# Optimization experiments

Hardware: AMD Instinct MI355X
Metric: run time of the kernel (lower is better)

## Reference

```python
import jax, jax.numpy as jnp
import numpy as np

FEATURE_DIM = 512
HIDDEN_DIM = 512
N_HEADS = 8
HEAD_DIM = HIDDEN_DIM // N_HEADS
MAX_LEN = 5000
GAMMA = 0.5  # gaussian relative-position bias width
LN_EPS = 1e-5


def make_pe(d_model, max_len):
    # sinusoidal positional encoding buffer, as in PositionalEncoding.__init__
    pos = jnp.arange(max_len, dtype=jnp.float32)[:, None]
    div = jnp.exp(jnp.arange(0, d_model, 2, dtype=jnp.float32) * (-np.log(10000.0) / d_model))
    ang = pos * div  # [max_len, d_model/2]
    pe = jnp.zeros((max_len, d_model), dtype=jnp.float32)
    pe = pe.at[:, 0::2].set(jnp.sin(ang)).at[:, 1::2].set(jnp.cos(ang))
    return pe


def setup_inputs() -> dict:
    key = jax.random.key(0)
    k_x, k_q, k_k, k_v = jax.random.split(key, 4)
    xavier = np.sqrt(6.0 / (FEATURE_DIM + HEAD_DIM))  # xavier_uniform over last two dims
    return {
        "data_window": jax.random.normal(k_x, (1, 2048, FEATURE_DIM), dtype=jnp.float32),
        "W_query": jax.random.uniform(k_q, (N_HEADS, FEATURE_DIM, HEAD_DIM), jnp.float32, -xavier, xavier),
        "W_key": jax.random.uniform(k_k, (N_HEADS, FEATURE_DIM, HEAD_DIM), jnp.float32, -xavier, xavier),
        "W_value": jax.random.uniform(k_v, (N_HEADS, FEATURE_DIM, HEAD_DIM), jnp.float32, -xavier, xavier),
        "ln_gamma": jnp.ones((FEATURE_DIM,), dtype=jnp.float32),
        "ln_beta": jnp.zeros((FEATURE_DIM,), dtype=jnp.float32),
    }


def reference(data_window, W_query, W_key, W_value, ln_gamma, ln_beta):
    B, S, F = data_window.shape
    temperature = 1.0

    # LayerNorm over feature dim
    mu = jnp.mean(data_window, axis=-1, keepdims=True)
    var = jnp.mean(jnp.square(data_window - mu), axis=-1, keepdims=True)
    x = (data_window - mu) * jax.lax.rsqrt(var + LN_EPS) * ln_gamma + ln_beta

    # positional encoding, exactly as original: x + pe[:x.shape[0]] (requires B==1)
    pe = make_pe(FEATURE_DIM, MAX_LEN)
    x = x + pe[:B]  # [B,F] broadcasts over [B,S,F] only because B==1

    # per-head QKV projections, vectorized over heads
    Q = jnp.einsum('bsf,hfd->bhsd', x, W_query)
    K = jnp.einsum('bsf,hfd->bhsd', x, W_key)
    V = jnp.einsum('bsf,hfd->bhsd', x, W_value)

    scores = jnp.einsum('bhsd,bhtd->bhst', Q, K) / np.sqrt(HEAD_DIM)

    # gaussian relative-position bias: scale(=1) * exp(-gamma * (i-j)^2)
    p = jnp.arange(S, dtype=jnp.float32)
    rel = p[:, None] - p[None, :]
    bias = jnp.exp(-GAMMA * jnp.square(rel))  # [S,S]
    scores = (scores + bias[None, None]) / temperature
    # dropout on scores is identity in eval mode

    attn = jax.nn.softmax(scores, axis=-1)  # [B,H,S,S]
    head_out = jnp.einsum('bhst,bhtd->bhsd', attn, V)

    # concat heads along feature dim: [B,S,H*D]
    multi_head_output = head_out.transpose(0, 2, 1, 3).reshape(B, S, N_HEADS * HEAD_DIM)
    mean_weights = jnp.mean(attn, axis=1)  # [B,S,S]
    return multi_head_output, mean_weights
```

## Files before the change

kernel.cpp:

```cpp
#include <hip/hip_runtime.h>
#include <hip/hip_bf16.h>
#include <math.h>

#define S_LEN 2048
#define FDIM  512
#define NH    8
#define HD    64
#define MH_ELEMS (S_LEN * FDIM)
#define MEAN_ELEMS (S_LEN * S_LEN)

typedef _Float16 half_t;
typedef _Float16 half2v __attribute__((ext_vector_type(2)));
typedef _Float16 half8v __attribute__((ext_vector_type(8)));
typedef float    float4v __attribute__((ext_vector_type(4)));

#define MFMA16(a, b, c) __builtin_amdgcn_mfma_f32_16x16x32_f16((a), (b), (c), 0, 0, 0)

__global__ __launch_bounds__(256) void ln_pe_kernel(const float* __restrict__ x,
                                                    const float* __restrict__ gamma,
                                                    const float* __restrict__ beta,
                                                    half_t* __restrict__ xo) {
    const int row = blockIdx.x;
    const int tid = threadIdx.x;
    const float2 v = ((const float2*)(x + (size_t)row * FDIM))[tid];
    float s = v.x + v.y;
    float q = v.x * v.x + v.y * v.y;
    #pragma unroll
    for (int off = 1; off < 64; off <<= 1) {
        s += __shfl_xor(s, off, 64);
        q += __shfl_xor(q, off, 64);
    }
    __shared__ float red[8];
    const int wave = tid >> 6;
    if ((tid & 63) == 0) { red[wave] = s; red[4 + wave] = q; }
    __syncthreads();
    s = red[0] + red[1] + red[2] + red[3];
    q = red[4] + red[5] + red[6] + red[7];
    const float mu  = s * (1.0f / FDIM);
    const float var = q * (1.0f / FDIM) - mu * mu;
    const float rstd = rsqrtf(var + 1e-5f);
    const int f0 = tid * 2, f1 = tid * 2 + 1;
    const float o0 = (v.x - mu) * rstd * gamma[f0] + beta[f0];
    const float o1 = (v.y - mu) * rstd * gamma[f1] + beta[f1] + 1.0f;
    half2v o; o.x = (half_t)o0; o.y = (half_t)o1;
    ((half2v*)(xo + (size_t)row * FDIM))[tid] = o;
}

__global__ __launch_bounds__(256) void qkv_kernel(const half_t* __restrict__ xh,
                                                  const float* __restrict__ Wq,
                                                  const float* __restrict__ Wk,
                                                  const float* __restrict__ Wv,
                                                  half_t* __restrict__ Qo,
                                                  half_t* __restrict__ Ko,
                                                  half_t* __restrict__ Vo) {
    const int ms0 = blockIdx.x * 128;
    const int h   = blockIdx.y;
    const int z   = blockIdx.z;
    const float* W = ((z == 0) ? Wq : (z == 1) ? Wk : Wv) + (size_t)h * FDIM * HD;
    half_t* Co = ((z == 0) ? Qo : (z == 1) ? Ko : Vo) + (size_t)h * S_LEN * HD;

    __shared__ half_t Xs[128][40];
    __shared__ half_t Wt[64][40];

    const int tid  = threadIdx.x;
    const int wv   = tid >> 6, lane = tid & 63;
    const int lo   = lane & 15, qq  = lane >> 4;

    const float4v zero4 = {0.f, 0.f, 0.f, 0.f};
    float4v acc[2][4];
    #pragma unroll
    for (int rg = 0; rg < 2; ++rg)
        #pragma unroll
        for (int cg = 0; cg < 4; ++cg) acc[rg][cg] = zero4;

    for (int k0 = 0; k0 < FDIM; k0 += 32) {
        #pragma unroll
        for (int it = 0; it < 2; ++it) {
            const int idx = tid + it * 256;
            const int r = idx >> 2, ch = idx & 3;
            *(half8v*)&Xs[r][ch * 8] = *(const half8v*)(xh + (size_t)(ms0 + r) * FDIM + k0 + ch * 8);
        }
        #pragma unroll
        for (int it = 0; it < 2; ++it) {
            const int idx = tid + it * 256;
            const int kr = idx >> 4, dc = idx & 15;
            const float4 w4 = *(const float4*)(W + (size_t)(k0 + kr) * HD + dc * 4);
            Wt[dc * 4 + 0][kr] = (half_t)w4.x;
            Wt[dc * 4 + 1][kr] = (half_t)w4.y;
            Wt[dc * 4 + 2][kr] = (half_t)w4.z;
            Wt[dc * 4 + 3][kr] = (half_t)w4.w;
        }
        __syncthreads();
        half8v a[2], b[4];
        #pragma unroll
        for (int rg = 0; rg < 2; ++rg) a[rg] = *(const half8v*)&Xs[wv * 32 + rg * 16 + lo][qq * 8];
        #pragma unroll
        for (int cg = 0; cg < 4; ++cg) b[cg] = *(const half8v*)&Wt[cg * 16 + lo][qq * 8];
        #pragma unroll
        for (int rg = 0; rg < 2; ++rg)
            #pragma unroll
            for (int cg = 0; cg < 4; ++cg) acc[rg][cg] = MFMA16(a[rg], b[cg], acc[rg][cg]);
        __syncthreads();
    }
    #pragma unroll
    for (int rg = 0; rg < 2; ++rg)
        #pragma unroll
        for (int cg = 0; cg < 4; ++cg)
            #pragma unroll
            for (int r = 0; r < 4; ++r)
                Co[(size_t)(ms0 + wv * 32 + rg * 16 + qq * 4 + r) * HD + cg * 16 + lo] =
                    (half_t)acc[rg][cg][r];
}

__global__ __launch_bounds__(256) void attn_kernel(const half_t* __restrict__ Qw,
                                                   const half_t* __restrict__ Kw,
                                                   const half_t* __restrict__ Vw,
                                                   half_t* __restrict__ Pg,
                                                   float* __restrict__ out,
                                                   const int use_p) {
    const int s0 = blockIdx.x * 32;
    const int h  = blockIdx.y;
    const half_t* Qh = Qw + (size_t)h * S_LEN * HD;
    const half_t* Kh = Kw + (size_t)h * S_LEN * HD;
    const half_t* Vh = Vw + (size_t)h * S_LEN * HD;

    __shared__ half_t Ks[128][72];
    __shared__ half_t Vt[64][136];
    __shared__ half_t Ps[32][136];
    __shared__ float  mred[2][32], lred[2][32];

    const int tid  = threadIdx.x;
    const int wv   = tid >> 6, lane = tid & 63;
    const int rg   = wv & 1,  ch    = wv >> 1;
    const int lo   = lane & 15, qq  = lane >> 4;

    half8v aq[2];
    #pragma unroll
    for (int kk = 0; kk < 2; ++kk)
        aq[kk] = *(const half8v*)(Qh + (size_t)(s0 + rg * 16 + lo) * HD + kk * 32 + qq * 8);

    float mrun[4], lrun[4];
    #pragma unroll
    for (int r = 0; r < 4; ++r) { mrun[r] = -1e30f; lrun[r] = 0.f; }

    for (int nt = 0; nt < 16; ++nt) {
        const int t0 = nt * 128;
        #pragma unroll
        for (int it = 0; it < 4; ++it) {
            const int idx = tid + it * 256;
            const int r = idx >> 3, c = idx & 7;
            *(half8v*)&Ks[r][c * 8] = *(const half8v*)(Kh + (size_t)(t0 + r) * HD + c * 8);
        }
        __syncthreads();
        float sv[4][4];
        #pragma unroll
        for (int ct = 0; ct < 4; ++ct) {
            const half8v b0 = *(const half8v*)&Ks[ch * 64 + ct * 16 + lo][qq * 8];
            const half8v b1 = *(const half8v*)&Ks[ch * 64 + ct * 16 + lo][32 + qq * 8];
            float4v c4 = {0.f, 0.f, 0.f, 0.f};
            c4 = MFMA16(aq[0], b0, c4);
            c4 = MFMA16(aq[1], b1, c4);
            const int colg = t0 + ch * 64 + ct * 16 + lo;
            #pragma unroll
            for (int r = 0; r < 4; ++r) {
                const float dd = (float)(s0 + rg * 16 + qq * 4 + r - colg);
                sv[ct][r] = c4[r] * 0.125f + __expf(-0.5f * dd * dd);
            }
        }
        #pragma unroll
        for (int r = 0; r < 4; ++r) {
            float tm = fmaxf(fmaxf(sv[0][r], sv[1][r]), fmaxf(sv[2][r], sv[3][r]));
            #pragma unroll
            for (int mk = 1; mk < 16; mk <<= 1) tm = fmaxf(tm, __shfl_xor(tm, mk, 64));
            const float mn  = fmaxf(mrun[r], tm);
            const float scl = __expf(mrun[r] - mn);
            float rs = 0.f;
            #pragma unroll
            for (int ct = 0; ct < 4; ++ct) rs += __expf(sv[ct][r] - mn);
            #pragma unroll
            for (int mk = 1; mk < 16; mk <<= 1) rs += __shfl_xor(rs, mk, 64);
            lrun[r] = lrun[r] * scl + rs;
            mrun[r] = mn;
        }
        __syncthreads();
    }

    if (lo == 0) {
        #pragma unroll
        for (int r = 0; r < 4; ++r) {
            mred[ch][rg * 16 + qq * 4 + r] = mrun[r];
            lred[ch][rg * 16 + qq * 4 + r] = lrun[r];
        }
    }
    __syncthreads();
    float mfin[4], minv[4];
    #pragma unroll
    for (int r = 0; r < 4; ++r) {
        const int row = rg * 16 + qq * 4 + r;
        const float m0 = mred[0][row], m1 = mred[1][row];
        const float mm = fmaxf(m0, m1);
        const float ll = lred[0][row] * __expf(m0 - mm) + lred[1][row] * __expf(m1 - mm);
        mfin[r] = mm; minv[r] = 1.f / ll;
    }
    __syncthreads();

    const float4v zero4 = {0.f, 0.f, 0.f, 0.f};
    float4v accO[2]; accO[0] = zero4; accO[1] = zero4;

    for (int nt = 0; nt < 16; ++nt) {
        const int t0 = nt * 128;
        #pragma unroll
        for (int it = 0; it < 4; ++it) {
            const int idx = tid + it * 256;
            const int r = idx >> 3, c = idx & 7;
            *(half8v*)&Ks[r][c * 8] = *(const half8v*)(Kh + (size_t)(t0 + r) * HD + c * 8);
        }
        #pragma unroll
        for (int it = 0; it < 4; ++it) {
            const int idx = tid + it * 256;
            const int t = idx >> 3, dc = idx & 7;
            const half8v v8 = *(const half8v*)(Vh + (size_t)(t0 + t) * HD + dc * 8);
            #pragma unroll
            for (int j = 0; j < 8; ++j) Vt[dc * 8 + j][t] = v8[j];
        }
        __syncthreads();
        #pragma unroll
        for (int ct = 0; ct < 4; ++ct) {
            const half8v b0 = *(const half8v*)&Ks[ch * 64 + ct * 16 + lo][qq * 8];
            const half8v b1 = *(const half8v*)&Ks[ch * 64 + ct * 16 + lo][32 + qq * 8];
            float4v c4 = {0.f, 0.f, 0.f, 0.f};
            c4 = MFMA16(aq[0], b0, c4);
            c4 = MFMA16(aq[1], b1, c4);
            const int colg = t0 + ch * 64 + ct * 16 + lo;
            #pragma unroll
            for (int r = 0; r < 4; ++r) {
                const float dd = (float)(s0 + rg * 16 + qq * 4 + r - colg);
                const float s = c4[r] * 0.125f + __expf(-0.5f * dd * dd);
                const float p = __expf(s - mfin[r]) * minv[r];
                Ps[rg * 16 + qq * 4 + r][ch * 64 + ct * 16 + lo] = (half_t)p;
            }
        }
        __syncthreads();
        {
            const int row = tid >> 3, cc = (tid & 7) * 16;
            const half8v p0 = *(const half8v*)&Ps[row][cc];
            const half8v p1 = *(const half8v*)&Ps[row][cc + 8];
            if (use_p) {
                half_t* dst = Pg + (size_t)h * MEAN_ELEMS + (size_t)(s0 + row) * S_LEN + t0 + cc;
                *(half8v*)dst = p0;
                *(half8v*)(dst + 8) = p1;
            } else {
                float* mo = out + MH_ELEMS + (size_t)(s0 + row) * S_LEN + t0 + cc;
                #pragma unroll
                for (int j = 0; j < 8; ++j) {
                    atomicAdd(mo + j,     (float)p0[j] * 0.125f);
                    atomicAdd(mo + 8 + j, (float)p1[j] * 0.125f);
                }
            }
        }
        #pragma unroll
        for (int ks = 0; ks < 4; ++ks) {
            const half8v ap = *(const half8v*)&Ps[rg * 16 + lo][ks * 32 + qq * 8];
            #pragma unroll
            for (int dgi = 0; dgi < 2; ++dgi) {
                const half8v bv = *(const half8v*)&Vt[(ch * 2 + dgi) * 16 + lo][ks * 32 + qq * 8];
                accO[dgi] = MFMA16(ap, bv, accO[dgi]);
            }
        }
        __syncthreads();
    }

    #pragma unroll
    for (int dgi = 0; dgi < 2; ++dgi)
        #pragma unroll
        for (int r = 0; r < 4; ++r)
            out[(size_t)(s0 + rg * 16 + qq * 4 + r) * FDIM + h * HD + (ch * 2 + dgi) * 16 + lo] =
                accO[dgi][r];
}

__global__ __launch_bounds__(256) void mean_kernel(const half_t* __restrict__ Pg,
                                                   float* __restrict__ out) {
    const size_t idx = ((size_t)blockIdx.x * 256 + threadIdx.x) * 8;
    float acc[8] = {0.f, 0.f, 0.f, 0.f, 0.f, 0.f, 0.f, 0.f};
    #pragma unroll
    for (int hh = 0; hh < NH; ++hh) {
        const half8v p = *(const half8v*)(Pg + (size_t)hh * MEAN_ELEMS + idx);
        #pragma unroll
        for (int j = 0; j < 8; ++j) acc[j] += (float)p[j];
    }
    float* o = out + MH_ELEMS + idx;
    *(float4*)o       = make_float4(acc[0] * 0.125f, acc[1] * 0.125f, acc[2] * 0.125f, acc[3] * 0.125f);
    *(float4*)(o + 4) = make_float4(acc[4] * 0.125f, acc[5] * 0.125f, acc[6] * 0.125f, acc[7] * 0.125f);
}

extern "C" void kernel_launch(void* const* d_in, const int* in_sizes, int n_in,
                              void* d_out, int out_size, void* d_ws, size_t ws_size,
                              hipStream_t stream) {
    const float* x  = (const float*)d_in[0];
    const float* Wq = (const float*)d_in[1];
    const float* Wk = (const float*)d_in[2];
    const float* Wv = (const float*)d_in[3];
    const float* g  = (const float*)d_in[4];
    const float* b  = (const float*)d_in[5];
    float* out = (float*)d_out;
    char*  ws  = (char*)d_ws;

    half_t* xh = (half_t*)(ws);
    half_t* Qh = (half_t*)(ws + (2ull << 20));
    half_t* Kh = (half_t*)(ws + (4ull << 20));
    half_t* Vh = (half_t*)(ws + (6ull << 20));
    half_t* Pg = (half_t*)(ws + (8ull << 20));
    const bool use_p = ws_size >= (72ull << 20);

    ln_pe_kernel<<<S_LEN, 256, 0, stream>>>(x, g, b, xh);
    qkv_kernel<<<dim3(16, 8, 3), 256, 0, stream>>>(xh, Wq, Wk, Wv, Qh, Kh, Vh);
    if (!use_p) {
        hipMemsetAsync(out + MH_ELEMS, 0, (size_t)MEAN_ELEMS * sizeof(float), stream);
    }
    attn_kernel<<<dim3(64, 8), 256, 0, stream>>>(Qh, Kh, Vh, Pg, out, use_p ? 1 : 0);
    if (use_p) {
        mean_kernel<<<MEAN_ELEMS / 8 / 256, 256, 0, stream>>>(Pg, out);
    }
}
```

Measured before the change: 191.0 us.

## Restructure attention: separate row-sum pass, head-looped column-split attention, fused mean

The softmax denominator now comes from a dedicated lsum kernel, and the running-max is replaced by a clamp at 60. The attention kernel splits the key dimension across blocks and loops over all heads inside each block, so the head-mean of the attention weights is accumulated in registers and written once. This removes the fp16 per-head P buffer and the separate mean kernel. Per-column-chunk partial outputs go to a workspace and a reduce kernel sums them. The QKV kernel also drops its shared-memory staging and reads operands straight from global memory. The costs are recomputing QK^T twice, the extra partial-output traffic, and numerical risk from dropping max subtraction.

Result: no change. 190.5 us (-0.3%).

```diff
diff --git a/kernel.cpp b/kernel.cpp
--- a/kernel.cpp
+++ b/kernel.cpp
@@ -11,10 +11,14 @@
 
 typedef _Float16 half_t;
 typedef _Float16 half2v __attribute__((ext_vector_type(2)));
+typedef _Float16 half4v __attribute__((ext_vector_type(4)));
 typedef _Float16 half8v __attribute__((ext_vector_type(8)));
 typedef float    float4v __attribute__((ext_vector_type(4)));
 
 #define MFMA16(a, b, c) __builtin_amdgcn_mfma_f32_16x16x32_f16((a), (b), (c), 0, 0, 0)
+
+#define VT_STRIDE 260
+#define PS_STRIDE 264
 
 __global__ __launch_bounds__(256) void ln_pe_kernel(const float* __restrict__ x,
                                                     const float* __restrict__ gamma,
@@ -59,12 +63,9 @@
     const float* W = ((z == 0) ? Wq : (z == 1) ? Wk : Wv) + (size_t)h * FDIM * HD;
     half_t* Co = ((z == 0) ? Qo : (z == 1) ? Ko : Vo) + (size_t)h * S_LEN * HD;
 
-    __shared__ half_t Xs[128][40];
-    __shared__ half_t Wt[64][40];
-
-    const int tid  = threadIdx.x;
-    const int wv   = tid >> 6, lane = tid & 63;
-    const int lo   = lane & 15, qq  = lane >> 4;
+    const int tid = threadIdx.x;
+    const int wv = tid >> 6, lane = tid & 63;
+    const int lo = lane & 15, qq = lane >> 4;
 
     const float4v zero4 = {0.f, 0.f, 0.f, 0.f};
     float4v acc[2][4];
@@ -74,33 +75,20 @@
         for (int cg = 0; cg < 4; ++cg) acc[rg][cg] = zero4;
 
     for (int k0 = 0; k0 < FDIM; k0 += 32) {
-        #pragma unroll
-        for (int it = 0; it < 2; ++it) {
-            const int idx = tid + it * 256;
-            const int r = idx >> 2, ch = idx & 3;
-            *(half8v*)&Xs[r][ch * 8] = *(const half8v*)(xh + (size_t)(ms0 + r) * FDIM + k0 + ch * 8);
-        }
-        #pragma unroll
-        for (int it = 0; it < 2; ++it) {
-            const int idx = tid + it * 256;
-            const int kr = idx >> 4, dc = idx & 15;
-            const float4 w4 = *(const float4*)(W + (size_t)(k0 + kr) * HD + dc * 4);
-            Wt[dc * 4 + 0][kr] = (half_t)w4.x;
-            Wt[dc * 4 + 1][kr] = (half_t)w4.y;
-            Wt[dc * 4 + 2][kr] = (half_t)w4.z;
-            Wt[dc * 4 + 3][kr] = (half_t)w4.w;
-        }
-        __syncthreads();
-        half8v a[2], b[4];
-        #pragma unroll
-        for (int rg = 0; rg < 2; ++rg) a[rg] = *(const half8v*)&Xs[wv * 32 + rg * 16 + lo][qq * 8];
-        #pragma unroll
-        for (int cg = 0; cg < 4; ++cg) b[cg] = *(const half8v*)&Wt[cg * 16 + lo][qq * 8];
+        half8v a[2];
         #pragma unroll
         for (int rg = 0; rg < 2; ++rg)
-            #pragma unroll
-            for (int cg = 0; cg < 4; ++cg) acc[rg][cg] = MFMA16(a[rg], b[cg], acc[rg][cg]);
-        __syncthreads();
+            a[rg] = *(const half8v*)(xh + (size_t)(ms0 + wv * 32 + rg * 16 + lo) * FDIM + k0 + qq * 8);
+        half8v bw[4];
+        #pragma unroll
+        for (int cg = 0; cg < 4; ++cg)
+            #pragma unroll
+            for (int j = 0; j < 8; ++j)
+                bw[cg][j] = (half_t)W[(size_t)(k0 + qq * 8 + j) * HD + cg * 16 + lo];
+        #pragma unroll
+        for (int rg = 0; rg < 2; ++rg)
+            #pragma unroll
+            for (int cg = 0; cg < 4; ++cg) acc[rg][cg] = MFMA16(a[rg], bw[cg], acc[rg][cg]);
     }
     #pragma unroll
     for (int rg = 0; rg < 2; ++rg)
@@ -112,185 +100,171 @@
                     (half_t)acc[rg][cg][r];
 }
 
-__global__ __launch_bounds__(256) void attn_kernel(const half_t* __restrict__ Qw,
+__global__ __launch_bounds__(256) void lsum_kernel(const half_t* __restrict__ Qw,
                                                    const half_t* __restrict__ Kw,
-                                                   const half_t* __restrict__ Vw,
-                                                   half_t* __restrict__ Pg,
-                                                   float* __restrict__ out,
-                                                   const int use_p) {
-    const int s0 = blockIdx.x * 32;
+                                                   float* __restrict__ linv) {
+    const int s0 = blockIdx.x * 16;
     const int h  = blockIdx.y;
     const half_t* Qh = Qw + (size_t)h * S_LEN * HD;
     const half_t* Kh = Kw + (size_t)h * S_LEN * HD;
-    const half_t* Vh = Vw + (size_t)h * S_LEN * HD;
-
-    __shared__ half_t Ks[128][72];
-    __shared__ half_t Vt[64][136];
-    __shared__ half_t Ps[32][136];
-    __shared__ float  mred[2][32], lred[2][32];
-
-    const int tid  = threadIdx.x;
-    const int wv   = tid >> 6, lane = tid & 63;
-    const int rg   = wv & 1,  ch    = wv >> 1;
-    const int lo   = lane & 15, qq  = lane >> 4;
-
-    half8v aq[2];
-    #pragma unroll
-    for (int kk = 0; kk < 2; ++kk)
-        aq[kk] = *(const half8v*)(Qh + (size_t)(s0 + rg * 16 + lo) * HD + kk * 32 + qq * 8);
-
-    float mrun[4], lrun[4];
-    #pragma unroll
-    for (int r = 0; r < 4; ++r) { mrun[r] = -1e30f; lrun[r] = 0.f; }
-
-    for (int nt = 0; nt < 16; ++nt) {
-        const int t0 = nt * 128;
-        #pragma unroll
-        for (int it = 0; it < 4; ++it) {
-            const int idx = tid + it * 256;
-            const int r = idx >> 3, c = idx & 7;
-            *(half8v*)&Ks[r][c * 8] = *(const half8v*)(Kh + (size_t)(t0 + r) * HD + c * 8);
-        }
+
+    const int tid = threadIdx.x;
+    const int wv = tid >> 6, lane = tid & 63;
+    const int lo = lane & 15, qq = lane >> 4;
+
+    const half8v aq0 = *(const half8v*)(Qh + (size_t)(s0 + lo) * HD + qq * 8);
+    const half8v aq1 = *(const half8v*)(Qh + (size_t)(s0 + lo) * HD + 32 + qq * 8);
+
+    float esum[4] = {0.f, 0.f, 0.f, 0.f};
+    for (int j = 0; j < 32; ++j) {
+        const int cbase = (wv + 4 * j) * 16;
+        const half8v b0 = *(const half8v*)(Kh + (size_t)(cbase + lo) * HD + qq * 8);
+        const half8v b1 = *(const half8v*)(Kh + (size_t)(cbase + lo) * HD + 32 + qq * 8);
+        float4v c4 = {0.f, 0.f, 0.f, 0.f};
+        c4 = MFMA16(aq0, b0, c4);
+        c4 = MFMA16(aq1, b1, c4);
+        const int dd0 = cbase - s0;
+        const bool near = (dd0 > -24) && (dd0 < 24);
+        #pragma unroll
+        for (int r = 0; r < 4; ++r) {
+            float s = c4[r] * 0.125f;
+            if (near) {
+                const float d = (float)(s0 + qq * 4 + r - cbase - lo);
+                s += __expf(-0.5f * d * d);
+            }
+            s = fminf(s, 60.f);
+            esum[r] += __expf(s);
+        }
+    }
+    #pragma unroll
+    for (int r = 0; r < 4; ++r) {
+        #pragma unroll
+        for (int mk = 1; mk < 16; mk <<= 1) esum[r] += __shfl_xor(esum[r], mk, 64);
+    }
+    __shared__ float red[4][16];
+    if (lo == 0) {
+        #pragma unroll
+        for (int r = 0; r < 4; ++r) red[wv][qq * 4 + r] = esum[r];
+    }
+    __syncthreads();
+    if (tid < 16) {
+        const float l = red[0][tid] + red[1][tid] + red[2][tid] + red[3][tid];
+        linv[(size_t)h * S_LEN + s0 + tid] = 1.0f / l;
+    }
+}
+
+__global__ __launch_bounds__(256, 3) void attn_kernel(const half_t* __restrict__ Qw,
+                                                      const half_t* __restrict__ Kw,
+                                                      const half_t* __restrict__ Vw,
+                                                      const float* __restrict__ linv,
+                                                      float* __restrict__ partial,
+                                                      float* __restrict__ out) {
+    const int s0 = blockIdx.x * 32;
+    const int c0 = blockIdx.y * 256;
+
+    __shared__ half_t Vt[64 * VT_STRIDE];
+    __shared__ half_t Ps[32 * PS_STRIDE];
+
+    const int tid = threadIdx.x;
+    const int wv = tid >> 6, lane = tid & 63;
+    const int rg = wv & 1, chw = wv >> 1;
+    const int lo = lane & 15, qq = lane >> 4;
+    const int rbase = s0 + rg * 16;
+    const int tlow = tid & 31, dcs = tid >> 5;
+
+    float msum[8][4];
+    #pragma unroll
+    for (int ct = 0; ct < 8; ++ct)
+        #pragma unroll
+        for (int r = 0; r < 4; ++r) msum[ct][r] = 0.f;
+
+    float* po = partial + (size_t)blockIdx.y * (size_t)MH_ELEMS;
+
+    for (int h = 0; h < NH; ++h) {
+        const half_t* Qh = Qw + (size_t)h * S_LEN * HD;
+        const half_t* Kh = Kw + (size_t)h * S_LEN * HD;
+        const half_t* Vh = Vw + (size_t)h * S_LEN * HD;
         __syncthreads();
-        float sv[4][4];
-        #pragma unroll
-        for (int ct = 0; ct < 4; ++ct) {
-            const half8v b0 = *(const half8v*)&Ks[ch * 64 + ct * 16 + lo][qq * 8];
-            const half8v b1 = *(const half8v*)&Ks[ch * 64 + ct * 16 + lo][32 + qq * 8];
+        #pragma unroll
+        for (int it = 0; it < 8; ++it) {
+            const int t = tlow + 32 * it;
+            const half8v v8 = *(const half8v*)(Vh + (size_t)(c0 + t) * HD + dcs * 8);
+            #pragma unroll
+            for (int j = 0; j < 8; ++j) Vt[(size_t)(dcs * 8 + j) * VT_STRIDE + t] = v8[j];
+        }
+        const half8v aq0 = *(const half8v*)(Qh + (size_t)(rbase + lo) * HD + qq * 8);
+        const half8v aq1 = *(const half8v*)(Qh + (size_t)(rbase + lo) * HD + 32 + qq * 8);
+        float li[4];
+        #pragma unroll
+        for (int r = 0; r < 4; ++r) li[r] = linv[(size_t)h * S_LEN + rbase + qq * 4 + r];
+        #pragma unroll
+        for (int ct = 0; ct < 8; ++ct) {
+            const int cbase = c0 + chw * 128 + ct * 16;
+            const half8v b0 = *(const half8v*)(Kh + (size_t)(cbase + lo) * HD + qq * 8);
+            const half8v b1 = *(const half8v*)(Kh + (size_t)(cbase + lo) * HD + 32 + qq * 8);
             float4v c4 = {0.f, 0.f, 0.f, 0.f};
-            c4 = MFMA16(aq[0], b0, c4);
-            c4 = MFMA16(aq[1], b1, c4);
-            const int colg = t0 + ch * 64 + ct * 16 + lo;
+            c4 = MFMA16(aq0, b0, c4);
+            c4 = MFMA16(aq1, b1, c4);
+            const int dd0 = cbase - rbase;
+            const bool near = (dd0 > -24) && (dd0 < 24);
             #pragma unroll
             for (int r = 0; r < 4; ++r) {
-                const float dd = (float)(s0 + rg * 16 + qq * 4 + r - colg);
-                sv[ct][r] = c4[r] * 0.125f + __expf(-0.5f * dd * dd);
+                float s = c4[r] * 0.125f;
+                if (near) {
+                    const float d = (float)(rbase + qq * 4 + r - cbase - lo);
+                    s += __expf(-0.5f * d * d);
+                }
+                s = fminf(s, 60.f);
+                const float e = __expf(s);
+                const float p = e * li[r];
+                msum[ct][r] += p;
+                Ps[(size_t)(rg * 16 + qq * 4 + r) * PS_STRIDE + chw * 128 + ct * 16 + lo] = (half_t)p;
             }
         }
-        #pragma unroll
-        for (int r = 0; r < 4; ++r) {
-            float tm = fmaxf(fmaxf(sv[0][r], sv[1][r]), fmaxf(sv[2][r], sv[3][r]));
-            #pragma unroll
-            for (int mk = 1; mk < 16; mk <<= 1) tm = fmaxf(tm, __shfl_xor(tm, mk, 64));
-            const float mn  = fmaxf(mrun[r], tm);
-            const float scl = __expf(mrun[r] - mn);
-            float rs = 0.f;
-            #pragma unroll
-            for (int ct = 0; ct < 4; ++ct) rs += __expf(sv[ct][r] - mn);
-            #pragma unroll
-            for (int mk = 1; mk < 16; mk <<= 1) rs += __shfl_xor(rs, mk, 64);
-            lrun[r] = lrun[r] * scl + rs;
-            mrun[r] = mn;
-        }
         __syncthreads();
-    }
-
-    if (lo == 0) {
-        #pragma unroll
-        for (int r = 0; r < 4; ++r) {
-            mred[ch][rg * 16 + qq * 4 + r] = mrun[r];
-            lred[ch][rg * 16 + qq * 4 + r] = lrun[r];
-        }
-    }
-    __syncthreads();
-    float mfin[4], minv[4];
-    #pragma unroll
-    for (int r = 0; r < 4; ++r) {
-        const int row = rg * 16 + qq * 4 + r;
-        const float m0 = mred[0][row], m1 = mred[1][row];
-        const float mm = fmaxf(m0, m1);
-        const float ll = lred[0][row] * __expf(m0 - mm) + lred[1][row] * __expf(m1 - mm);
-        mfin[r] = mm; minv[r] = 1.f / ll;
-    }
-    __syncthreads();
-
-    const float4v zero4 = {0.f, 0.f, 0.f, 0.f};
-    float4v accO[2]; accO[0] = zero4; accO[1] = zero4;
-
-    for (int nt = 0; nt < 16; ++nt) {
-        const int t0 = nt * 128;
-        #pragma unroll
-        for (int it = 0; it < 4; ++it) {
-            const int idx = tid + it * 256;
-            const int r = idx >> 3, c = idx & 7;
-            *(half8v*)&Ks[r][c * 8] = *(const half8v*)(Kh + (size_t)(t0 + r) * HD + c * 8);
-        }
-        #pragma unroll
-        for (int it = 0; it < 4; ++it) {
-            const int idx = tid + it * 256;
-            const int t = idx >> 3, dc = idx & 7;
-            const half8v v8 = *(const half8v*)(Vh + (size_t)(t0 + t) * HD + dc * 8);
-            #pragma unroll
-            for (int j = 0; j < 8; ++j) Vt[dc * 8 + j][t] = v8[j];
-        }
-        __syncthreads();
-        #pragma unroll
-        for (int ct = 0; ct < 4; ++ct) {
-            const half8v b0 = *(const half8v*)&Ks[ch * 64 + ct * 16 + lo][qq * 8];
-            const half8v b1 = *(const half8v*)&Ks[ch * 64 + ct * 16 + lo][32 + qq * 8];
-            float4v c4 = {0.f, 0.f, 0.f, 0.f};
-            c4 = MFMA16(aq[0], b0, c4);
-            c4 = MFMA16(aq[1], b1, c4);
-            const int colg = t0 + ch * 64 + ct * 16 + lo;
-            #pragma unroll
-            for (int r = 0; r < 4; ++r) {
-                const float dd = (float)(s0 + rg * 16 + qq * 4 + r - colg);
-                const float s = c4[r] * 0.125f + __expf(-0.5f * dd * dd);
-                const float p = __expf(s - mfin[r]) * minv[r];
-                Ps[rg * 16 + qq * 4 + r][ch * 64 + ct * 16 + lo] = (half_t)p;
-            }
-        }
-        __syncthreads();
-        {
-            const int row = tid >> 3, cc = (tid & 7) * 16;
-            const half8v p0 = *(const half8v*)&Ps[row][cc];
-            const half8v p1 = *(const half8v*)&Ps[row][cc + 8];
-            if (use_p) {
-                half_t* dst = Pg + (size_t)h * MEAN_ELEMS + (size_t)(s0 + row) * S_LEN + t0 + cc;
-                *(half8v*)dst = p0;
-                *(half8v*)(dst + 8) = p1;
-            } else {
-                float* mo = out + MH_ELEMS + (size_t)(s0 + row) * S_LEN + t0 + cc;
-                #pragma unroll
-                for (int j = 0; j < 8; ++j) {
-                    atomicAdd(mo + j,     (float)p0[j] * 0.125f);
-                    atomicAdd(mo + 8 + j, (float)p1[j] * 0.125f);
-                }
-            }
-        }
-        #pragma unroll
-        for (int ks = 0; ks < 4; ++ks) {
-            const half8v ap = *(const half8v*)&Ps[rg * 16 + lo][ks * 32 + qq * 8];
+        float4v accO[2];
+        accO[0] = (float4v){0.f, 0.f, 0.f, 0.f};
+        accO[1] = (float4v){0.f, 0.f, 0.f, 0.f};
+        #pragma unroll
+        for (int ks = 0; ks < 8; ++ks) {
+            const half8v ap = *(const half8v*)&Ps[(size_t)(rg * 16 + lo) * PS_STRIDE + ks * 32 + qq * 8];
             #pragma unroll
             for (int dgi = 0; dgi < 2; ++dgi) {
-                const half8v bv = *(const half8v*)&Vt[(ch * 2 + dgi) * 16 + lo][ks * 32 + qq * 8];
+                const int d0 = (chw * 2 + dgi) * 16;
+                const size_t voff = (size_t)(d0 + lo) * VT_STRIDE + ks * 32 + qq * 8;
+                const half4v u0 = *(const half4v*)&Vt[voff];
+                const half4v u1 = *(const half4v*)&Vt[voff + 4];
+                half8v bv;
+                bv[0] = u0[0]; bv[1] = u0[1]; bv[2] = u0[2]; bv[3] = u0[3];
+                bv[4] = u1[0]; bv[5] = u1[1]; bv[6] = u1[2]; bv[7] = u1[3];
                 accO[dgi] = MFMA16(ap, bv, accO[dgi]);
             }
         }
-        __syncthreads();
-    }
-
-    #pragma unroll
-    for (int dgi = 0; dgi < 2; ++dgi)
+        #pragma unroll
+        for (int dgi = 0; dgi < 2; ++dgi)
+            #pragma unroll
+            for (int r = 0; r < 4; ++r)
+                po[(size_t)(rbase + qq * 4 + r) * FDIM + h * HD + (chw * 2 + dgi) * 16 + lo] =
+                    accO[dgi][r];
+    }
+    #pragma unroll
+    for (int ct = 0; ct < 8; ++ct)
         #pragma unroll
         for (int r = 0; r < 4; ++r)
-            out[(size_t)(s0 + rg * 16 + qq * 4 + r) * FDIM + h * HD + (ch * 2 + dgi) * 16 + lo] =
-                accO[dgi][r];
-}
-
-__global__ __launch_bounds__(256) void mean_kernel(const half_t* __restrict__ Pg,
-                                                   float* __restrict__ out) {
-    const size_t idx = ((size_t)blockIdx.x * 256 + threadIdx.x) * 8;
-    float acc[8] = {0.f, 0.f, 0.f, 0.f, 0.f, 0.f, 0.f, 0.f};
-    #pragma unroll
-    for (int hh = 0; hh < NH; ++hh) {
-        const half8v p = *(const half8v*)(Pg + (size_t)hh * MEAN_ELEMS + idx);
-        #pragma unroll
-        for (int j = 0; j < 8; ++j) acc[j] += (float)p[j];
-    }
-    float* o = out + MH_ELEMS + idx;
-    *(float4*)o       = make_float4(acc[0] * 0.125f, acc[1] * 0.125f, acc[2] * 0.125f, acc[3] * 0.125f);
-    *(float4*)(o + 4) = make_float4(acc[4] * 0.125f, acc[5] * 0.125f, acc[6] * 0.125f, acc[7] * 0.125f);
+            out[MH_ELEMS + (size_t)(rbase + qq * 4 + r) * S_LEN + c0 + chw * 128 + ct * 16 + lo] =
+                msum[ct][r] * 0.125f;
+}
+
+__global__ __launch_bounds__(256) void reduce_kernel(const float* __restrict__ partial,
+                                                     float* __restrict__ out) {
+    const size_t i4 = ((size_t)blockIdx.x * 256 + threadIdx.x) * 4;
+    float4 s = *(const float4*)(partial + i4);
+    #pragma unroll
+    for (int c = 1; c < 8; ++c) {
+        const float4 t = *(const float4*)(partial + (size_t)c * MH_ELEMS + i4);
+        s.x += t.x; s.y += t.y; s.z += t.z; s.w += t.w;
+    }
+    *(float4*)(out + i4) = s;
 }
 
 extern "C" void kernel_launch(void* const* d_in, const int* in_sizes, int n_in,
@@ -305,20 +279,16 @@
     float* out = (float*)d_out;
     char*  ws  = (char*)d_ws;
 
-    half_t* xh = (half_t*)(ws);
-    half_t* Qh = (half_t*)(ws + (2ull << 20));
-    half_t* Kh = (half_t*)(ws + (4ull << 20));
-    half_t* Vh = (half_t*)(ws + (6ull << 20));
-    half_t* Pg = (half_t*)(ws + (8ull << 20));
-    const bool use_p = ws_size >= (72ull << 20);
+    half_t* xh   = (half_t*)(ws);
+    half_t* Qh   = (half_t*)(ws + (2ull << 20));
+    half_t* Kh   = (half_t*)(ws + (4ull << 20));
+    half_t* Vh   = (half_t*)(ws + (6ull << 20));
+    float*  linv = (float*)(ws + (8ull << 20));
+    float*  part = (float*)(ws + (9ull << 20));
 
     ln_pe_kernel<<<S_LEN, 256, 0, stream>>>(x, g, b, xh);
     qkv_kernel<<<dim3(16, 8, 3), 256, 0, stream>>>(xh, Wq, Wk, Wv, Qh, Kh, Vh);
-    if (!use_p) {
-        hipMemsetAsync(out + MH_ELEMS, 0, (size_t)MEAN_ELEMS * sizeof(float), stream);
-    }
-    attn_kernel<<<dim3(64, 8), 256, 0, stream>>>(Qh, Kh, Vh, Pg, out, use_p ? 1 : 0);
-    if (use_p) {
-        mean_kernel<<<MEAN_ELEMS / 8 / 256, 256, 0, stream>>>(Pg, out);
-    }
-}
+    lsum_kernel<<<dim3(128, 8), 256, 0, stream>>>(Qh, Kh, linv);
+    attn_kernel<<<dim3(64, 8), 256, 0, stream>>>(Qh, Kh, Vh, linv, part, out);
+    reduce_kernel<<<MH_ELEMS / 4 / 256, 256, 0, stream>>>(part, out);
+}
```
